# Kernel optimization log

Hardware: AMD Instinct MI355X
Metric: run time of the kernel (lower is better)

The kernel has to match this reference:

```python
import math
import jax, jax.numpy as jnp
import numpy as np

FNUM = 64      # exp_channels (fnum)
NHEADS = 4     # num_heads
WS = 8         # window size (both spatial dims)
SHIFT = 4      # cyclic shift (hard-coded in module)
SCALE = FNUM ** -0.5   # NOTE: module scales by fnum**-0.5, not head_dim**-0.5
LN_EPS = 1e-5


def sine_pos_encoding(h, w, num_pos_feats, temperature=10000.0):
    # DETR-style normalized sine position encoding -> (1, h*w, 2*num_pos_feats)
    scale = 2.0 * math.pi
    y = np.cumsum(np.ones((1, h, w), dtype=np.float64), axis=1)
    x = np.cumsum(np.ones((1, h, w), dtype=np.float64), axis=2)
    eps = 1e-6
    y = y / (y[:, -1:, :] + eps) * scale
    x = x / (x[:, :, -1:] + eps) * scale
    dim_t = np.arange(num_pos_feats, dtype=np.float64)
    dim_t = temperature ** (2.0 * (dim_t // 2) / num_pos_feats)
    pos_x = x[..., None] / dim_t
    pos_y = y[..., None] / dim_t
    pos_x = np.stack([np.sin(pos_x[..., 0::2]), np.cos(pos_x[..., 1::2])], axis=-1).reshape(1, h, w, -1)
    pos_y = np.stack([np.sin(pos_y[..., 0::2]), np.cos(pos_y[..., 1::2])], axis=-1).reshape(1, h, w, -1)
    pos = np.concatenate([pos_y, pos_x], axis=-1)
    return jnp.asarray(pos.reshape(1, h * w, 2 * num_pos_feats), dtype=jnp.float32)


def compute_mask_np(H, W, ws, ss):
    # Swin shifted-window attention mask -> (nW, ws*ws, ws*ws) with 0 / -100
    img = np.zeros((H, W))
    cnt = 0
    for hs in (slice(0, -ws), slice(-ws, -ss), slice(-ss, None)):
        for wsl in (slice(0, -ws), slice(-ws, -ss), slice(-ss, None)):
            img[hs, wsl] = cnt
            cnt += 1
    mw = img.reshape(H // ws, ws, W // ws, ws).transpose(0, 2, 1, 3).reshape(-1, ws * ws)
    diff = mw[:, None, :] - mw[:, :, None]
    return jnp.asarray(np.where(diff != 0, -100.0, 0.0), dtype=jnp.float32)


def layernorm(x, w, b):
    m = x.mean(-1, keepdims=True)
    v = x.var(-1, keepdims=True)
    return (x - m) * jax.lax.rsqrt(v + LN_EPS) * w + b


def window_attention(q, k, v, mask):
    # q,k,v: (Bw, nH, N, Ch); mask: (nW, N, N)
    att = jnp.einsum('bhnc,bhmc->bhnm', q * SCALE, k)
    nW, N = mask.shape[0], mask.shape[1]
    att = att.reshape(-1, nW, NHEADS, N, N) + mask[None, :, None]
    att = jax.nn.softmax(att.reshape(-1, NHEADS, N, N), axis=-1)
    out = jnp.einsum('bhnm,bhmc->bnhc', att, v)   # merge heads as (nH C)
    return out.reshape(out.shape[0], N, -1)


def merge_heads(q):
    # (Bw, nH, N, Ch) -> (Bw, N, nH*Ch)
    return q.transpose(0, 2, 1, 3).reshape(q.shape[0], q.shape[2], -1)


def geglu(h, w11, b11, w12, b12, w2, b2):
    return (jax.nn.gelu(h @ w11 + b11, approximate=False) * (h @ w12 + b12)) @ w2 + b2


def reference(x, ln1_w, ln1_b, ln2_w, ln2_b, w_qkv, me_w11, me_b11, me_w12, me_b12, me_w2, me_b2, conv11_w, ff_in_w, ff_dw_w, ff_out_w):
    B, _, C, H, W = x.shape
    nHw, nWw = H // WS, W // WS
    nW = nHw * nWw
    N = WS * WS
    Ch = FNUM // NHEADS
    pos = sine_pos_encoding(WS, WS, FNUM // 2)
    mask = compute_mask_np(H, W, WS, SHIFT)
    x0 = x
    xs = jnp.roll(x, (-SHIFT, -SHIFT), axis=(3, 4))
    # window partition: (B,3,C,H,W) -> (B*3*nW, N, C)
    xw = xs.reshape(B, 3, C, nHw, WS, nWw, WS).transpose(0, 1, 3, 5, 4, 6, 2).reshape(-1, N, C)
    xw = layernorm(xw, ln1_w, ln1_b)
    qkv = (xw + pos) @ w_qkv                                   # (B*3*nW, N, 3F)
    # '(B E nW) W (nP C) -> E nP (B nW) W C'
    qkv = qkv.reshape(B, 3, nW, N, 3, FNUM).transpose(1, 4, 0, 2, 3, 5).reshape(3, 3, B * nW, N, FNUM)
    # '(C nH)' head split: head index is the fast axis (faithful to source)
    qkv = qkv.reshape(3, 3, B * nW, N, Ch, NHEADS).transpose(0, 1, 2, 5, 3, 4)  # (E, P, Bw, nH, N, Ch)
    a1 = window_attention(qkv[1, 0], qkv[0, 1], qkv[0, 2], mask)
    a3 = window_attention(qkv[1, 0], qkv[2, 1], qkv[2, 2], mask)
    a21 = window_attention(qkv[0, 0], qkv[1, 1], qkv[1, 2], mask)
    a21b = window_attention(qkv[0, 0], qkv[2, 1], qkv[2, 2], mask)
    a23 = window_attention(qkv[2, 0], qkv[1, 1], qkv[1, 2], mask)
    a23b = window_attention(qkv[2, 0], qkv[0, 1], qkv[0, 2], mask)
    # keep_query=True path: concat attended features with own query, GEGLU per exposure
    h1 = geglu(jnp.concatenate([a21, a21b, merge_heads(qkv[0, 0])], -1), me_w11[0], me_b11[0], me_w12[0], me_b12[0], me_w2[0], me_b2[0])
    h2 = geglu(jnp.concatenate([a1, a3, merge_heads(qkv[1, 0])], -1), me_w11[1], me_b11[1], me_w12[1], me_b12[1], me_w2[1], me_b2[1])
    h3 = geglu(jnp.concatenate([a23, a23b, merge_heads(qkv[2, 0])], -1), me_w11[2], me_b11[2], me_w12[2], me_b12[2], me_w2[2], me_b2[2])
    xc = jnp.concatenate([h1, h2, h3], 0)                      # (3*B*nW, N, F)
    # window reverse + ffn_dconv 1x1 conv across 3F channels
    xr = xc.reshape(3, B, nHw, nWw, WS, WS, FNUM).transpose(1, 0, 6, 2, 4, 3, 5).reshape(B, 3 * FNUM, H, W)
    xr = jnp.einsum('oi,bihw->bohw', conv11_w, xr).reshape(B, 3, FNUM, H, W)
    xr = jnp.roll(xr, (SHIFT, SHIFT), axis=(3, 4))
    xres = xr + x0
    # FFN: LN over (N C), then GEGLU dwconv FeedForward
    xl = layernorm(xres.transpose(0, 3, 4, 1, 2).reshape(B, H, W, 3 * FNUM), ln2_w, ln2_b)
    xcn = xl.transpose(0, 3, 1, 2)                             # (B, 3F, H, W)
    h = jnp.einsum('oi,bihw->bohw', ff_in_w, xcn)              # (B, 12F, H, W)
    h = jax.lax.conv_general_dilated(h, ff_dw_w[:, None], (1, 1), ((1, 1), (1, 1)),
                                     feature_group_count=h.shape[1],
                                     dimension_numbers=('NCHW', 'OIHW', 'NCHW'))
    g1, g2 = jnp.split(h, 2, axis=1)
    h = jax.nn.gelu(g1, approximate=False) * g2                # (B, 6F, H, W)
    out = jnp.einsum('oi,bihw->bohw', ff_out_w, h).reshape(B, 3, FNUM, H, W)
    return xres + out


def setup_inputs():
    key = jax.random.key(0)
    ks = jax.random.split(key, 10)
    F3, F6, F12 = 3 * FNUM, 6 * FNUM, 12 * FNUM
    def w(k, shape, fan_in):
        return jax.random.normal(k, shape, jnp.float32) * (fan_in ** -0.5)
    return {
        'x': jax.random.normal(ks[0], (1, 3, FNUM, 256, 256), jnp.float32),
        'ln1_w': jnp.ones((FNUM,), jnp.float32),
        'ln1_b': jnp.zeros((FNUM,), jnp.float32),
        'ln2_w': jnp.ones((F3,), jnp.float32),
        'ln2_b': jnp.zeros((F3,), jnp.float32),
        'w_qkv': w(ks[1], (FNUM, F3), FNUM),
        'me_w11': w(ks[2], (3, F3, FNUM), F3),
        'me_b11': jnp.zeros((3, FNUM), jnp.float32),
        'me_w12': w(ks[3], (3, F3, FNUM), F3),
        'me_b12': jnp.zeros((3, FNUM), jnp.float32),
        'me_w2': w(ks[4], (3, FNUM, FNUM), FNUM),
        'me_b2': jnp.zeros((3, FNUM), jnp.float32),
        'conv11_w': w(ks[5], (F3, F3), F3),
        'ff_in_w': w(ks[6], (F12, F3), F3),
        'ff_dw_w': w(ks[7], (F12, 3, 3), 9),
        'ff_out_w': w(ks[8], (F3, F6), F6),
    }
```

## Files before the change

### kernel.cpp

```cpp
#include <hip/hip_runtime.h>
#include <hip/hip_bf16.h>
#include <math.h>

typedef __hip_bfloat16 bf16;
typedef __attribute__((ext_vector_type(8))) short short8;
typedef __attribute__((ext_vector_type(4))) short short4v;
typedef __attribute__((ext_vector_type(4))) float f32x4;

__device__ __forceinline__ float b2f(bf16 v) { return __bfloat162float(v); }
__device__ __forceinline__ bf16 f2b(float v) { return __float2bfloat16(v); }
__device__ __forceinline__ short f2s(float v) { bf16 b = __float2bfloat16(v); return *(short*)&b; }
__device__ __forceinline__ float s2f(short s) { bf16 b = *(bf16*)&s; return __bfloat162float(b); }
__device__ __forceinline__ float gelu_exact(float x) {
  return 0.5f * x * (1.0f + erff(x * 0.7071067811865476f));
}
__device__ __forceinline__ bool detect_f32(const void* ln1w) {
  return *(const unsigned int*)ln1w == 0x3F800000u;
}
__device__ __forceinline__ float ldx(const void* p, int i, bool f32) {
  return f32 ? ((const float*)p)[i] : b2f(((const bf16*)p)[i]);
}
#define MFMA16(a, b, c) __builtin_amdgcn_mfma_f32_16x16x32_bf16((a), (b), (c), 0, 0, 0)

#define OFF_LN1W  0
#define OFF_LN1B  64
#define OFF_LN2W  128
#define OFF_LN2B  320
#define OFF_WQKVT 512
#define OFF_W11T  12800
#define OFF_B11   49664
#define OFF_W12T  49856
#define OFF_B12   86720
#define OFF_W2T   86912
#define OFF_B2    99200
#define OFF_CW    99392
#define OFF_FIW   136256
#define OFF_DWW   283712
#define OFF_FOW   290624

#define QOFF 0
#define KOFF 4352
#define VOFF 9472

__global__ void __launch_bounds__(256) k_convert(
    const void* __restrict__ src, bf16* __restrict__ dst, int n,
    const void* __restrict__ raw) {
  const bool f32 = detect_f32(raw);
  int i = blockIdx.x * 256 + threadIdx.x;
  if (i < n) dst[i] = f2b(ldx(src, i, f32));
}

__global__ void __launch_bounds__(256) k_convT(
    const void* __restrict__ src, bf16* __restrict__ dst, int R, int C, int n,
    const void* __restrict__ raw) {
  const bool f32 = detect_f32(raw);
  int i = blockIdx.x * 256 + threadIdx.x;
  if (i >= n) return;
  int rc = R * C;
  int s = i / rc, rem = i - s * rc;
  int r = rem / C, c = rem - r * C;
  dst[s * rc + c * R + r] = f2b(ldx(src, i, f32));
}

__global__ void __launch_bounds__(256) k_pos(float* __restrict__ posT) {
  int i = blockIdx.x * 256 + threadIdx.x;
  if (i >= 4096) return;
  int t = i >> 6, ch = i & 63;
  int r = t >> 3, c = t & 7;
  int c2 = ch & 31;
  float coord = (ch < 32) ? (float)(r + 1) : (float)(c + 1);
  float base = coord * (6.283185307179586f / 8.000001f);
  int k = c2 >> 1;
  float d = powf(10000.0f, (float)k * (1.0f / 16.0f));
  float a = base / d;
  posT[i] = (c2 & 1) ? cosf(a) : sinf(a);
}

__global__ void __launch_bounds__(256) k_qkv(
    const void* __restrict__ x, const void* __restrict__ raw,
    const bf16* __restrict__ W, const float* __restrict__ posT,
    short* __restrict__ qkvS, int wy0, int NWL) {
  const int wl = blockIdx.x;
  const int wy = wy0 + (wl >> 5), wx = wl & 31;
  const int tid = threadIdx.x;
  const bool xf32 = detect_f32(raw);

  __shared__ alignas(16) short xln[192 * 72];
  __shared__ alignas(16) short qout[13824];
  __shared__ float mu[192], rs[192];

  for (int i = tid; i < 3072; i += 256) {
    int xq = i & 1, ty = (i >> 1) & 7, ch = (i >> 4) & 63, e = i >> 10;
    int y  = (wy * 8 + ty + 4) & 255;
    int xs = (wx * 8 + 4 + xq * 4) & 255;
    size_t gi = ((size_t)(e * 64 + ch) * 256 + y) * 256 + xs;
    float f0, f1, f2, f3;
    if (xf32) {
      f32x4 v4 = *(const f32x4*)((const float*)x + gi);
      f0 = v4[0]; f1 = v4[1]; f2 = v4[2]; f3 = v4[3];
    } else {
      short4v v4 = *(const short4v*)((const bf16*)x + gi);
      f0 = s2f(v4[0]); f1 = s2f(v4[1]); f2 = s2f(v4[2]); f3 = s2f(v4[3]);
    }
    int tb = (e * 64 + ty * 8 + xq * 4) * 72 + ch;
    xln[tb]       = f2s(f0);
    xln[tb + 72]  = f2s(f1);
    xln[tb + 144] = f2s(f2);
    xln[tb + 216] = f2s(f3);
  }
  __syncthreads();
  if (tid < 192) {
    const short* row = xln + tid * 72;
    float s = 0.f, s2 = 0.f;
    #pragma unroll
    for (int k8 = 0; k8 < 8; k8++) {
      short8 v = *(const short8*)(row + k8 * 8);
      #pragma unroll
      for (int j = 0; j < 8; j++) { float f = s2f(v[j]); s += f; s2 += f * f; }
    }
    float m = s * (1.0f / 64.0f);
    float var = s2 * (1.0f / 64.0f) - m * m;
    mu[tid] = m; rs[tid] = rsqrtf(var + 1e-5f);
  }
  __syncthreads();
  for (int u = tid; u < 1536; u += 256) {
    int co = u & 7, t = (u >> 3) & 63, e = u >> 9;
    int idx = (e * 64 + t) * 72 + co * 8;
    short8 xv = *(const short8*)(xln + idx);
    float m = mu[e * 64 + t], rr = rs[e * 64 + t];
    const float* pt = posT + t * 64 + co * 8;
    f32x4 pa = *(const f32x4*)pt;
    f32x4 pb = *(const f32x4*)(pt + 4);
    short8 lw = *(const short8*)(const void*)(W + OFF_LN1W + co * 8);
    short8 lb = *(const short8*)(const void*)(W + OFF_LN1B + co * 8);
    short8 o;
    #pragma unroll
    for (int j = 0; j < 8; j++) {
      float p = (j < 4) ? pa[j] : pb[j - 4];
      o[j] = f2s((s2f(xv[j]) - m) * rr * s2f(lw[j]) + s2f(lb[j]) + p);
    }
    *(short8*)(xln + idx) = o;
  }
  __syncthreads();

  const int lid = tid & 63;
  const int w = tid >> 6;
  const int mrow = lid & 15, q = lid >> 4;
  const int t0 = w * 16 + q * 4;
  const int h = mrow & 3;
  const bf16* wqT = W + OFF_WQKVT;
  for (int e = 0; e < 3; e++) {
    short8 a0 = *(const short8*)(xln + (e * 64 + w * 16 + mrow) * 72 + q * 8);
    short8 a1 = *(const short8*)(xln + (e * 64 + w * 16 + mrow) * 72 + 32 + q * 8);
    for (int nt = 0; nt < 12; nt++) {
      f32x4 acc = {0.f, 0.f, 0.f, 0.f};
      short8 b0 = *(const short8*)(const void*)(wqT + (nt * 16 + mrow) * 64 + q * 8);
      short8 b1 = *(const short8*)(const void*)(wqT + (nt * 16 + mrow) * 64 + 32 + q * 8);
      acc = MFMA16(a0, b0, acc);
      acc = MFMA16(a1, b1, acc);
      int p = nt >> 2;
      int c = (nt & 3) * 4 + (mrow >> 2);
      if (p == 0) {
        int o2 = h * 16 + c;
        #pragma unroll
        for (int r = 0; r < 4; r++)
          qout[QOFF + (t0 + r) * 68 + o2] = f2s(acc[r]);
      } else if (p == 1) {
        int rb = KOFF + (h * 64 + t0) * 20 + c;
        #pragma unroll
        for (int r = 0; r < 4; r++)
          qout[rb + r * 20] = f2s(acc[r] * 0.125f);
      } else {
        int rb = VOFF + (h * 16 + c) * 68 + q * 16 + w;
        #pragma unroll
        for (int r = 0; r < 4; r++)
          qout[rb + r * 4] = f2s(acc[r]);
      }
    }
    __syncthreads();
    const size_t gb = ((size_t)wl * 9 + e * 3) * 4096;
    for (int u = tid; u < 3072; u += 256) {
      int j = u * 4, p = j >> 12, rem = j & 4095, src;
      if (p == 0)      src = QOFF + (rem >> 6) * 68 + (rem & 63);
      else if (p == 1) src = KOFF + (rem >> 4) * 20 + (rem & 15);
      else             src = VOFF + (rem >> 6) * 68 + (rem & 63);
      *(short4v*)(qkvS + gb + j) = *(const short4v*)(qout + src);
    }
    __syncthreads();
  }
}

__global__ void __launch_bounds__(256, 3) k_attn(
    const short* __restrict__ qkvS, const bf16* __restrict__ W,
    short* __restrict__ xcS, int wy0, int NWL) {
  const int e  = blockIdx.x / NWL;
  const int wl = blockIdx.x - e * NWL;
  const int wy = wy0 + (wl >> 5), wx = wl & 31;
  const int tid = threadIdx.x;

  __shared__ alignas(16) short cat[64 * 200];
  __shared__ alignas(16) short Kh[4096];
  __shared__ alignas(16) short Vt[64 * 72];
  __shared__ alignas(16) short Pb[64 * 72];
  __shared__ alignas(16) short kz[16];
  short* gbuf = Pb;

  const int ea = (e == 0) ? 1 : ((e == 1) ? 0 : 1);
  const int eb = (e == 0) ? 2 : ((e == 1) ? 2 : 0);
  const short* Qg = qkvS + ((size_t)wl * 9 + e * 3 + 0) * 4096;
  const short* Kg[2] = { qkvS + ((size_t)wl * 9 + ea * 3 + 1) * 4096,
                         qkvS + ((size_t)wl * 9 + eb * 3 + 1) * 4096 };
  const short* Vg[2] = { qkvS + ((size_t)wl * 9 + ea * 3 + 2) * 4096,
                         qkvS + ((size_t)wl * 9 + eb * 3 + 2) * 4096 };

  if (tid < 16) kz[tid] = 0;
  for (int i = tid; i < 512; i += 256) {
    int t = i >> 3, ch = i & 7;
    *(short8*)(cat + t * 200 + 128 + ch * 8) = *(const short8*)(Qg + t * 64 + ch * 8);
  }

  const int lid = tid & 63;
  const int w = tid >> 6;
  const int mrow = lid & 15, q = lid >> 4;
  const int masky = (wy == 31), maskx = (wx == 31);
  const bool anymask = (masky | maskx) != 0;
  const short8 zero8 = {0, 0, 0, 0, 0, 0, 0, 0};

  float madd[4][4];
  if (anymask) {
    int qi = w * 16 + mrow;
    int lyi = masky ? (((qi >> 3) < 4) ? 1 : 2) : 0;
    int lxi = maskx ? (((qi & 7) < 4) ? 1 : 2) : 0;
    #pragma unroll
    for (int nt = 0; nt < 4; nt++)
      #pragma unroll
      for (int r = 0; r < 4; r++) {
        int kj = nt * 16 + q * 4 + r;
        int lyj = masky ? (((kj >> 3) < 4) ? 1 : 2) : 0;
        int lxj = maskx ? (((kj & 7) < 4) ? 1 : 2) : 0;
        madd[nt][r] = (lyi != lyj || lxi != lxj) ? -100.0f : 0.0f;
      }
  }

  for (int src = 0; src < 2; src++) {
    if (src) __syncthreads();
    for (int i = tid; i < 512; i += 256)
      *(short8*)(Kh + i * 8) = *(const short8*)(Kg[src] + i * 8);
    for (int i = tid; i < 512; i += 256) {
      int row = i >> 3, ch = i & 7;
      *(short8*)(Vt + row * 72 + ch * 8) = *(const short8*)(Vg[src] + row * 64 + ch * 8);
    }
    __syncthreads();

    for (int h = 0; h < 4; h++) {
      short8 qf = (q < 2)
          ? *(const short8*)(cat + (w * 16 + mrow) * 200 + 128 + h * 16 + q * 8)
          : zero8;
      const short* kb; int kstep;
      if (q < 2) { kb = Kh + (h * 64 + mrow) * 16 + q * 8; kstep = 256; }
      else       { kb = kz; kstep = 0; }
      f32x4 s[4];
      #pragma unroll
      for (int nt = 0; nt < 4; nt++) {
        short8 kf = *(const short8*)(kb + nt * kstep);
        f32x4 z = {0.f, 0.f, 0.f, 0.f};
        s[nt] = MFMA16(kf, qf, z);
      }
      if (anymask) {
        #pragma unroll
        for (int nt = 0; nt < 4; nt++)
          #pragma unroll
          for (int r = 0; r < 4; r++) s[nt][r] += madd[nt][r];
      }
      float mx = s[0][0];
      #pragma unroll
      for (int nt = 0; nt < 4; nt++)
        #pragma unroll
        for (int r = 0; r < 4; r++) if (nt | r) mx = fmaxf(mx, s[nt][r]);
      mx = fmaxf(mx, __shfl_xor(mx, 16));
      mx = fmaxf(mx, __shfl_xor(mx, 32));
      float pr[4][4]; float sum = 0.f;
      #pragma unroll
      for (int nt = 0; nt < 4; nt++)
        #pragma unroll
        for (int r = 0; r < 4; r++) {
          float ev = __expf(s[nt][r] - mx);
          pr[nt][r] = ev; sum += ev;
        }
      sum += __shfl_xor(sum, 16);
      sum += __shfl_xor(sum, 32);
      float inv = 1.0f / sum;
      int ro = (w * 16 + mrow) * 72 + q * 16;
      #pragma unroll
      for (int r = 0; r < 4; r++) {
        short4v pv = { f2s(pr[0][r] * inv), f2s(pr[1][r] * inv),
                       f2s(pr[2][r] * inv), f2s(pr[3][r] * inv) };
        *(short4v*)(Pb + ro + r * 4) = pv;
      }
      asm volatile("s_waitcnt lgkmcnt(0)" ::: "memory");
      f32x4 o = {0.f, 0.f, 0.f, 0.f};
      #pragma unroll
      for (int kc = 0; kc < 2; kc++) {
        short8 pa = *(const short8*)(Pb + (w * 16 + mrow) * 72 + kc * 32 + q * 8);
        short8 vb = *(const short8*)(Vt + (h * 16 + mrow) * 72 + kc * 32 + q * 8);
        o = MFMA16(pa, vb, o);
      }
      #pragma unroll
      for (int r = 0; r < 4; r++)
        cat[(w * 16 + q * 4 + r) * 200 + src * 64 + h * 16 + mrow] = f2s(o[r]);
    }
  }
  __syncthreads();

  {
    short8 a[6];
    #pragma unroll
    for (int kc = 0; kc < 6; kc++)
      a[kc] = *(const short8*)(cat + (w * 16 + mrow) * 200 + kc * 32 + q * 8);
    f32x4 ua[4], va[4];
    const bf16* w1T = W + OFF_W11T + (size_t)e * 64 * 192;
    const bf16* w2T = W + OFF_W12T + (size_t)e * 64 * 192;
    for (int nt = 0; nt < 4; nt++) {
      f32x4 au = {0.f, 0.f, 0.f, 0.f}, av = {0.f, 0.f, 0.f, 0.f};
      #pragma unroll
      for (int kc = 0; kc < 6; kc++) {
        short8 bu = *(const short8*)(const void*)(w1T + (nt * 16 + mrow) * 192 + kc * 32 + q * 8);
        short8 bv = *(const short8*)(const void*)(w2T + (nt * 16 + mrow) * 192 + kc * 32 + q * 8);
        au = MFMA16(a[kc], bu, au);
        av = MFMA16(a[kc], bv, av);
      }
      ua[nt] = au; va[nt] = av;
    }
    for (int nt = 0; nt < 4; nt++) {
      int o = nt * 16 + mrow;
      float bu = b2f(W[OFF_B11 + e * 64 + o]);
      float bv = b2f(W[OFF_B12 + e * 64 + o]);
      #pragma unroll
      for (int r = 0; r < 4; r++)
        gbuf[(w * 16 + q * 4 + r) * 72 + o] = f2s(gelu_exact(ua[nt][r] + bu) * (va[nt][r] + bv));
    }
  }
  {
    short8 g0 = *(const short8*)(gbuf + (w * 16 + mrow) * 72 + q * 8);
    short8 g1 = *(const short8*)(gbuf + (w * 16 + mrow) * 72 + 32 + q * 8);
    const bf16* w2T = W + OFF_W2T + (size_t)e * 64 * 64;
    for (int nt = 0; nt < 4; nt++) {
      f32x4 acc = {0.f, 0.f, 0.f, 0.f};
      short8 b0 = *(const short8*)(const void*)(w2T + (nt * 16 + mrow) * 64 + q * 8);
      short8 b1 = *(const short8*)(const void*)(w2T + (nt * 16 + mrow) * 64 + 32 + q * 8);
      acc = MFMA16(g0, b0, acc);
      acc = MFMA16(g1, b1, acc);
      int o = nt * 16 + mrow;
      float bb = b2f(W[OFF_B2 + e * 64 + o]);
      #pragma unroll
      for (int r = 0; r < 4; r++)
        cat[(w * 16 + q * 4 + r) * 200 + o] = f2s(acc[r] + bb);
    }
  }
  __syncthreads();
  short* xcbase = xcS + ((size_t)wl * 3 + e) * 4096;
  for (int i = tid; i < 1024; i += 256) {
    int tt = i >> 4, f4 = (i & 15) * 4;
    *(short4v*)(xcbase + tt * 64 + f4) = *(const short4v*)(cat + tt * 200 + f4);
  }
}

__global__ void __launch_bounds__(256) k_conv11(
    const short* __restrict__ xcS, const bf16* __restrict__ W,
    const void* __restrict__ x, const void* __restrict__ raw,
    short* __restrict__ xres, int wy0, int NWL) {
  const int wl = blockIdx.x;
  const int wy = wy0 + (wl >> 5), wx = wl & 31;
  const int tid = threadIdx.x;
  const bool xf32 = detect_f32(raw);
  __shared__ alignas(16) short ct[64 * 200];
  __shared__ alignas(16) short xt[64 * 200];

  for (int i = tid; i < 3072; i += 256) {
    int e = i >> 10, rem = i & 1023;
    int tt = rem >> 4, f4 = (rem & 15) * 4;
    *(short4v*)(ct + tt * 200 + e * 64 + f4)
        = *(const short4v*)(xcS + ((size_t)wl * 3 + e) * 4096 + tt * 64 + f4);
  }
  for (int i = tid; i < 3072; i += 256) {
    int xq = i & 1, ty = (i >> 1) & 7, ch = (i >> 4) & 63, e = i >> 10;
    int y  = (wy * 8 + ty + 4) & 255;
    int xs = (wx * 8 + 4 + xq * 4) & 255;
    size_t gi = ((size_t)(e * 64 + ch) * 256 + y) * 256 + xs;
    float f0, f1, f2, f3;
    if (xf32) {
      f32x4 v4 = *(const f32x4*)((const float*)x + gi);
      f0 = v4[0]; f1 = v4[1]; f2 = v4[2]; f3 = v4[3];
    } else {
      short4v v4 = *(const short4v*)((const bf16*)x + gi);
      f0 = s2f(v4[0]); f1 = s2f(v4[1]); f2 = s2f(v4[2]); f3 = s2f(v4[3]);
    }
    int tb = (ty * 8 + xq * 4) * 200 + e * 64 + ch;
    xt[tb]       = f2s(f0);
    xt[tb + 200] = f2s(f1);
    xt[tb + 400] = f2s(f2);
    xt[tb + 600] = f2s(f3);
  }
  __syncthreads();

  const int lid = tid & 63;
  const int w = tid >> 6;
  const int mrow = lid & 15, q = lid >> 4;
  short8 a[6];
  #pragma unroll
  for (int kc = 0; kc < 6; kc++)
    a[kc] = *(const short8*)(ct + (w * 16 + mrow) * 200 + kc * 32 + q * 8);
  __syncthreads();

  const bf16* cw = W + OFF_CW;
  for (int nt = 0; nt < 12; nt++) {
    f32x4 acc = {0.f, 0.f, 0.f, 0.f};
    #pragma unroll
    for (int kc = 0; kc < 6; kc++) {
      short8 b = *(const short8*)(const void*)(cw + (nt * 16 + mrow) * 192 + kc * 32 + q * 8);
      acc = MFMA16(a[kc], b, acc);
    }
    int o = nt * 16 + mrow;
    #pragma unroll
    for (int r = 0; r < 4; r++) {
      int t = w * 16 + q * 4 + r;
      ct[t * 200 + o] = f2s(acc[r] + s2f(xt[t * 200 + o]));
    }
  }
  __syncthreads();
  for (int i4 = tid; i4 < 3072; i4 += 256) {
    int t = i4 / 48, o4 = (i4 - t * 48) * 4;
    int y  = (wy * 8 + (t >> 3) + 4) & 255;
    int xx = (wx * 8 + (t & 7) + 4) & 255;
    *(short4v*)(xres + (size_t)(y * 256 + xx) * 192 + o4)
        = *(const short4v*)(ct + t * 200 + o4);
  }
}

__global__ void __launch_bounds__(256) k_ffin(
    const short* __restrict__ xres, const bf16* __restrict__ W,
    short* __restrict__ hS, int y_start, int y0m1) {
  const int y = y_start + (blockIdx.x >> 2);
  const int x0 = (blockIdx.x & 3) * 64;
  const int l = y - y0m1;
  const int tid = threadIdx.x;
  __shared__ alignas(16) short xt[64 * 200];
  __shared__ float mu[64], rs[64];

  for (int i4 = tid; i4 < 3072; i4 += 256) {
    int p = i4 / 48, c4 = (i4 - p * 48) * 4;
    *(short4v*)(xt + p * 200 + c4)
        = *(const short4v*)(xres + (size_t)(y * 256 + x0 + p) * 192 + c4);
  }
  __syncthreads();
  {
    int p = tid >> 2, qd = tid & 3;
    const short* row = xt + p * 200 + qd * 48;
    float s = 0.f, s2 = 0.f;
    #pragma unroll
    for (int k = 0; k < 6; k++) {
      short8 v = *(const short8*)(row + k * 8);
      #pragma unroll
      for (int j = 0; j < 8; j++) { float f = s2f(v[j]); s += f; s2 += f * f; }
    }
    s  += __shfl_xor(s, 1);  s  += __shfl_xor(s, 2);
    s2 += __shfl_xor(s2, 1); s2 += __shfl_xor(s2, 2);
    if (qd == 0) {
      float m = s * (1.0f / 192.0f);
      float var = s2 * (1.0f / 192.0f) - m * m;
      mu[p] = m; rs[p] = rsqrtf(var + 1e-5f);
    }
  }
  __syncthreads();
  for (int i = tid; i < 12288; i += 256) {
    int p = i & 63, ch = i >> 6;
    int idx = p * 200 + ch;
    xt[idx] = f2s((s2f(xt[idx]) - mu[p]) * rs[p] * b2f(W[OFF_LN2W + ch]) + b2f(W[OFF_LN2B + ch]));
  }
  __syncthreads();

  const int lid = tid & 63;
  const int m0 = (tid >> 6) * 16;
  const int mrow = lid & 15, q = lid >> 4;
  short8 a[6];
  #pragma unroll
  for (int kc = 0; kc < 6; kc++)
    a[kc] = *(const short8*)(xt + (m0 + mrow) * 200 + kc * 32 + q * 8);
  __syncthreads();

  const bf16* fiw = W + OFF_FIW;
  for (int c = 0; c < 4; c++) {
    for (int j = 0; j < 12; j++) {
      int nt = c * 12 + j;
      f32x4 acc = {0.f, 0.f, 0.f, 0.f};
      #pragma unroll
      for (int kc = 0; kc < 6; kc++) {
        short8 b = *(const short8*)(const void*)(fiw + (nt * 16 + mrow) * 192 + kc * 32 + q * 8);
        acc = MFMA16(a[kc], b, acc);
      }
      #pragma unroll
      for (int r = 0; r < 4; r++)
        xt[(m0 + q * 4 + r) * 200 + j * 16 + mrow] = f2s(acc[r]);
    }
    __syncthreads();
    for (int i4 = tid; i4 < 3072; i4 += 256) {
      int t = i4 / 48, o4 = (i4 - t * 48) * 4;
      *(short4v*)(hS + (size_t)l * 196608 + (size_t)(x0 + t) * 768 + c * 192 + o4)
          = *(const short4v*)(xt + t * 200 + o4);
    }
    __syncthreads();
  }
}

__global__ void __launch_bounds__(256, 3) k_ffout(
    const short* __restrict__ hS, const bf16* __restrict__ W,
    const short* __restrict__ xres, void* __restrict__ out,
    const void* __restrict__ raw, int y0, int y0m1) {
  const int y = y0 + (blockIdx.x >> 2);
  const int x0 = (blockIdx.x & 3) * 64;
  const int tid = threadIdx.x;
  const bool of32 = detect_f32(raw);
  __shared__ alignas(16) short ga[64 * 392];

  const bf16* dwwT = W + OFF_DWW;
  const int l = y - y0m1;
  const short8 z8 = {0, 0, 0, 0, 0, 0, 0, 0};
  for (int it = 0; it < 3; it++) {
    int unit = it * 256 + tid;
    int pq = unit / 48, oo = unit - pq * 48;
    int o = oo * 8;
    int xxb = x0 + pq * 4;
    float u[4][8], v[4][8];
    #pragma unroll
    for (int t4 = 0; t4 < 4; t4++)
      #pragma unroll
      for (int j = 0; j < 8; j++) { u[t4][j] = 0.f; v[t4][j] = 0.f; }
    #pragma unroll
    for (int dy = -1; dy <= 1; dy++) {
      int yy = y + dy;
      if (yy < 0 || yy >= 256) continue;
      const short* rbase = hS + (size_t)(l + dy) * 196608;
      short8 hu[6], hv[6];
      #pragma unroll
      for (int k = 0; k < 6; k++) {
        int xv = xxb - 1 + k;
        if (xv < 0 || xv >= 256) { hu[k] = z8; hv[k] = z8; }
        else {
          const short* hp = rbase + (size_t)xv * 768 + o;
          hu[k] = *(const short8*)(hp);
          hv[k] = *(const short8*)(hp + 384);
        }
      }
      const bf16* wrow = dwwT + (dy + 1) * 3 * 768 + o;
      short8 w0u = *(const short8*)(const void*)(wrow);
      short8 w0v = *(const short8*)(const void*)(wrow + 384);
      short8 w1u = *(const short8*)(const void*)(wrow + 768);
      short8 w1v = *(const short8*)(const void*)(wrow + 768 + 384);
      short8 w2u = *(const short8*)(const void*)(wrow + 1536);
      short8 w2v = *(const short8*)(const void*)(wrow + 1536 + 384);
      #pragma unroll
      for (int j = 0; j < 8; j++) {
        float a0 = s2f(w0u[j]), a1 = s2f(w1u[j]), a2 = s2f(w2u[j]);
        float b0 = s2f(w0v[j]), b1 = s2f(w1v[j]), b2 = s2f(w2v[j]);
        float fu0 = s2f(hu[0][j]), fu1 = s2f(hu[1][j]), fu2 = s2f(hu[2][j]);
        float fu3 = s2f(hu[3][j]), fu4 = s2f(hu[4][j]), fu5 = s2f(hu[5][j]);
        float fv0 = s2f(hv[0][j]), fv1 = s2f(hv[1][j]), fv2 = s2f(hv[2][j]);
        float fv3 = s2f(hv[3][j]), fv4 = s2f(hv[4][j]), fv5 = s2f(hv[5][j]);
        u[0][j] += a0 * fu0 + a1 * fu1 + a2 * fu2;
        u[1][j] += a0 * fu1 + a1 * fu2 + a2 * fu3;
        u[2][j] += a0 * fu2 + a1 * fu3 + a2 * fu4;
        u[3][j] += a0 * fu3 + a1 * fu4 + a2 * fu5;
        v[0][j] += b0 * fv0 + b1 * fv1 + b2 * fv2;
        v[1][j] += b0 * fv1 + b1 * fv2 + b2 * fv3;
        v[2][j] += b0 * fv2 + b1 * fv3 + b2 * fv4;
        v[3][j] += b0 * fv3 + b1 * fv4 + b2 * fv5;
      }
    }
    #pragma unroll
    for (int t4 = 0; t4 < 4; t4++) {
      short8 g;
      #pragma unroll
      for (int j = 0; j < 8; j++) g[j] = f2s(gelu_exact(u[t4][j]) * v[t4][j]);
      *(short8*)(ga + (pq * 4 + t4) * 392 + o) = g;
    }
  }
  __syncthreads();

  const int lid = tid & 63;
  const int m0 = (tid >> 6) * 16;
  const int mrow = lid & 15, q = lid >> 4;
  short8 a[12];
  #pragma unroll
  for (int kc = 0; kc < 12; kc++)
    a[kc] = *(const short8*)(ga + (m0 + mrow) * 392 + kc * 32 + q * 8);
  __syncthreads();

  for (int i4 = tid; i4 < 3072; i4 += 256) {
    int pp = i4 / 48, c4 = (i4 - pp * 48) * 4;
    *(short4v*)(ga + pp * 392 + 200 + c4)
        = *(const short4v*)(xres + (size_t)(y * 256 + x0 + pp) * 192 + c4);
  }

  const bf16* fow = W + OFF_FOW;
  for (int nt = 0; nt < 12; nt++) {
    f32x4 acc = {0.f, 0.f, 0.f, 0.f};
    #pragma unroll
    for (int kc = 0; kc < 12; kc++) {
      short8 b = *(const short8*)(const void*)(fow + (nt * 16 + mrow) * 384 + kc * 32 + q * 8);
      acc = MFMA16(a[kc], b, acc);
    }
    #pragma unroll
    for (int r = 0; r < 4; r++)
      ga[(m0 + q * 4 + r) * 392 + nt * 16 + mrow] = f2s(acc[r]);
  }
  __syncthreads();

  for (int it = 0; it < 48; it++) {
    int flat = it * 256 + tid;
    int pp = flat & 63, ch = flat >> 6;
    int idx = ch * 65536 + y * 256 + x0 + pp;
    float r = s2f(ga[pp * 392 + ch]) + s2f(ga[pp * 392 + 200 + ch]);
    if (of32) ((float*)out)[idx] = r;
    else      ((bf16*)out)[idx] = f2b(r);
  }
}

extern "C" void kernel_launch(void* const* d_in, const int* in_sizes, int n_in,
                              void* d_out, int out_size, void* d_ws, size_t ws_size,
                              hipStream_t stream) {
  const void* x   = d_in[0];
  const void* raw = d_in[1];
  char* ws = (char*)d_ws;
  bf16*  W    = (bf16*)(ws + 1024);
  float* posT = (float*)(ws + 786432);
  short* xres = (short*)(ws + 0x100000);
  const size_t ATT = 28ull * 1024 * 1024;

  size_t avail = (ws_size > ATT) ? ws_size - ATT : 0;
  int swr = 32;
  while (swr > 1 && (size_t)swr * 3145728ull > avail) swr >>= 1;
  int hr = 256;
  while (hr > 4 && (size_t)(hr + 2) * 393216ull > avail) hr >>= 1;

  short* qkvS = (short*)(ws + ATT);
  short* xcS  = (short*)(ws + ATT + (size_t)swr * 2359296ull);
  short* hS   = (short*)(ws + ATT);

  { const int di[10]   = {1, 2, 3, 4, 7, 9, 11, 12, 13, 15};
    const int offp[10] = {OFF_LN1W, OFF_LN1B, OFF_LN2W, OFF_LN2B, OFF_B11,
                          OFF_B12, OFF_B2, OFF_CW, OFF_FIW, OFF_FOW};
    const int cnt[10]  = {64, 64, 192, 192, 192, 192, 192, 36864, 147456, 73728};
    for (int i = 0; i < 10; i++)
      k_convert<<<(cnt[i] + 255) / 256, 256, 0, stream>>>(
          d_in[di[i]], W + offp[i], cnt[i], raw);
  }
  k_convT<<<(12288 + 255) / 256, 256, 0, stream>>>(d_in[5], W + OFF_WQKVT, 64, 192, 12288, raw);
  k_convT<<<(36864 + 255) / 256, 256, 0, stream>>>(d_in[6], W + OFF_W11T, 192, 64, 36864, raw);
  k_convT<<<(36864 + 255) / 256, 256, 0, stream>>>(d_in[8], W + OFF_W12T, 192, 64, 36864, raw);
  k_convT<<<(12288 + 255) / 256, 256, 0, stream>>>(d_in[10], W + OFF_W2T, 64, 64, 12288, raw);
  k_convT<<<(6912 + 255) / 256, 256, 0, stream>>>(d_in[14], W + OFF_DWW, 768, 9, 6912, raw);
  k_pos<<<16, 256, 0, stream>>>(posT);

  for (int wy0 = 0; wy0 < 32; wy0 += swr) {
    int NWL = swr * 32;
    k_qkv<<<NWL, 256, 0, stream>>>(x, raw, W, posT, qkvS, wy0, NWL);
    k_attn<<<3 * NWL, 256, 0, stream>>>(qkvS, W, xcS, wy0, NWL);
    k_conv11<<<NWL, 256, 0, stream>>>(xcS, W, x, raw, xres, wy0, NWL);
  }

  for (int y0 = 0; y0 < 256; y0 += hr) {
    int ys = (y0 == 0) ? 0 : (y0 - 1);
    int ye = (y0 + hr > 255) ? 255 : (y0 + hr);
    int nrows = ye - ys + 1;
    k_ffin<<<nrows * 4, 256, 0, stream>>>(xres, W, hS, ys, y0 - 1);
    k_ffout<<<hr * 4, 256, 0, stream>>>(hS, W, xres, d_out, raw, y0, y0 - 1);
  }
}
```

Baseline: 757.4 us.

## Use tanh GELU, fp32 depthwise weights, and 2-pixel strips in ffout

Replaces the exact erf GELU with a tanh-approximation built on __expf, in both the MoE gate and the feed-forward output kernel. Depthwise conv weights are now stored as transposed fp32, so bf16 unpacking of weights goes away. The depthwise loop computes 2 output pixels per thread over 6 iterations instead of 4 over 3, which lowers register pressure, and the explicit 3-blocks-per-CU launch bound is dropped. The trade-offs are more redundant halo loads and a GELU approximation that differs slightly from the reference erf form.

```diff
diff --git a/kernel.cpp b/kernel.cpp
--- a/kernel.cpp
+++ b/kernel.cpp
@@ -11,8 +11,11 @@
 __device__ __forceinline__ bf16 f2b(float v) { return __float2bfloat16(v); }
 __device__ __forceinline__ short f2s(float v) { bf16 b = __float2bfloat16(v); return *(short*)&b; }
 __device__ __forceinline__ float s2f(short s) { bf16 b = *(bf16*)&s; return __bfloat162float(b); }
-__device__ __forceinline__ float gelu_exact(float x) {
-  return 0.5f * x * (1.0f + erff(x * 0.7071067811865476f));
+__device__ __forceinline__ float gelu_fast(float x) {
+  float z = 0.7978845608028654f * x * (1.0f + 0.044715f * x * x);
+  float e = __expf(2.0f * z);
+  float t = 1.0f - 2.0f / (e + 1.0f);
+  return 0.5f * x * (1.0f + t);
 }
 __device__ __forceinline__ bool detect_f32(const void* ln1w) {
   return *(const unsigned int*)ln1w == 0x3F800000u;
@@ -35,7 +38,6 @@
 #define OFF_B2    99200
 #define OFF_CW    99392
 #define OFF_FIW   136256
-#define OFF_DWW   283712
 #define OFF_FOW   290624
 
 #define QOFF 0
@@ -60,6 +62,16 @@
   int s = i / rc, rem = i - s * rc;
   int r = rem / C, c = rem - r * C;
   dst[s * rc + c * R + r] = f2b(ldx(src, i, f32));
+}
+
+__global__ void __launch_bounds__(256) k_convTF(
+    const void* __restrict__ src, float* __restrict__ dst, int R, int C, int n,
+    const void* __restrict__ raw) {
+  const bool f32 = detect_f32(raw);
+  int i = blockIdx.x * 256 + threadIdx.x;
+  if (i >= n) return;
+  int r = i / C, c = i - r * C;
+  dst[c * R + r] = ldx(src, i, f32);
 }
 
 __global__ void __launch_bounds__(256) k_pos(float* __restrict__ posT) {
@@ -337,7 +349,7 @@
       float bv = b2f(W[OFF_B12 + e * 64 + o]);
       #pragma unroll
       for (int r = 0; r < 4; r++)
-        gbuf[(w * 16 + q * 4 + r) * 72 + o] = f2s(gelu_exact(ua[nt][r] + bu) * (va[nt][r] + bv));
+        gbuf[(w * 16 + q * 4 + r) * 72 + o] = f2s(gelu_fast(ua[nt][r] + bu) * (va[nt][r] + bv));
     }
   }
   {
@@ -512,8 +524,9 @@
   }
 }
 
-__global__ void __launch_bounds__(256, 3) k_ffout(
+__global__ void __launch_bounds__(256) k_ffout(
     const short* __restrict__ hS, const bf16* __restrict__ W,
+    const float* __restrict__ dwwF,
     const short* __restrict__ xres, void* __restrict__ out,
     const void* __restrict__ raw, int y0, int y0m1) {
   const int y = y0 + (blockIdx.x >> 2);
@@ -522,27 +535,23 @@
   const bool of32 = detect_f32(raw);
   __shared__ alignas(16) short ga[64 * 392];
 
-  const bf16* dwwT = W + OFF_DWW;
   const int l = y - y0m1;
   const short8 z8 = {0, 0, 0, 0, 0, 0, 0, 0};
-  for (int it = 0; it < 3; it++) {
+  for (int it = 0; it < 6; it++) {
     int unit = it * 256 + tid;
     int pq = unit / 48, oo = unit - pq * 48;
     int o = oo * 8;
-    int xxb = x0 + pq * 4;
-    float u[4][8], v[4][8];
-    #pragma unroll
-    for (int t4 = 0; t4 < 4; t4++)
-      #pragma unroll
-      for (int j = 0; j < 8; j++) { u[t4][j] = 0.f; v[t4][j] = 0.f; }
+    int xxb = x0 + pq * 2;
+    float u0[8] = {0,0,0,0,0,0,0,0}, v0[8] = {0,0,0,0,0,0,0,0};
+    float u1[8] = {0,0,0,0,0,0,0,0}, v1[8] = {0,0,0,0,0,0,0,0};
     #pragma unroll
     for (int dy = -1; dy <= 1; dy++) {
       int yy = y + dy;
       if (yy < 0 || yy >= 256) continue;
       const short* rbase = hS + (size_t)(l + dy) * 196608;
-      short8 hu[6], hv[6];
-      #pragma unroll
-      for (int k = 0; k < 6; k++) {
+      short8 hu[4], hv[4];
+      #pragma unroll
+      for (int k = 0; k < 4; k++) {
         int xv = xxb - 1 + k;
         if (xv < 0 || xv >= 256) { hu[k] = z8; hv[k] = z8; }
         else {
@@ -551,38 +560,27 @@
           hv[k] = *(const short8*)(hp + 384);
         }
       }
-      const bf16* wrow = dwwT + (dy + 1) * 3 * 768 + o;
-      short8 w0u = *(const short8*)(const void*)(wrow);
-      short8 w0v = *(const short8*)(const void*)(wrow + 384);
-      short8 w1u = *(const short8*)(const void*)(wrow + 768);
-      short8 w1v = *(const short8*)(const void*)(wrow + 768 + 384);
-      short8 w2u = *(const short8*)(const void*)(wrow + 1536);
-      short8 w2v = *(const short8*)(const void*)(wrow + 1536 + 384);
+      const float* wrow = dwwF + (dy + 1) * 3 * 768 + o;
       #pragma unroll
       for (int j = 0; j < 8; j++) {
-        float a0 = s2f(w0u[j]), a1 = s2f(w1u[j]), a2 = s2f(w2u[j]);
-        float b0 = s2f(w0v[j]), b1 = s2f(w1v[j]), b2 = s2f(w2v[j]);
-        float fu0 = s2f(hu[0][j]), fu1 = s2f(hu[1][j]), fu2 = s2f(hu[2][j]);
-        float fu3 = s2f(hu[3][j]), fu4 = s2f(hu[4][j]), fu5 = s2f(hu[5][j]);
-        float fv0 = s2f(hv[0][j]), fv1 = s2f(hv[1][j]), fv2 = s2f(hv[2][j]);
-        float fv3 = s2f(hv[3][j]), fv4 = s2f(hv[4][j]), fv5 = s2f(hv[5][j]);
-        u[0][j] += a0 * fu0 + a1 * fu1 + a2 * fu2;
-        u[1][j] += a0 * fu1 + a1 * fu2 + a2 * fu3;
-        u[2][j] += a0 * fu2 + a1 * fu3 + a2 * fu4;
-        u[3][j] += a0 * fu3 + a1 * fu4 + a2 * fu5;
-        v[0][j] += b0 * fv0 + b1 * fv1 + b2 * fv2;
-        v[1][j] += b0 * fv1 + b1 * fv2 + b2 * fv3;
-        v[2][j] += b0 * fv2 + b1 * fv3 + b2 * fv4;
-        v[3][j] += b0 * fv3 + b1 * fv4 + b2 * fv5;
-      }
-    }
-    #pragma unroll
-    for (int t4 = 0; t4 < 4; t4++) {
-      short8 g;
-      #pragma unroll
-      for (int j = 0; j < 8; j++) g[j] = f2s(gelu_exact(u[t4][j]) * v[t4][j]);
-      *(short8*)(ga + (pq * 4 + t4) * 392 + o) = g;
-    }
+        float a0 = wrow[j],          a1 = wrow[768 + j],       a2 = wrow[1536 + j];
+        float b0 = wrow[384 + j],    b1 = wrow[768 + 384 + j], b2 = wrow[1536 + 384 + j];
+        float h0u = s2f(hu[0][j]), h1u = s2f(hu[1][j]), h2u = s2f(hu[2][j]), h3u = s2f(hu[3][j]);
+        float h0v = s2f(hv[0][j]), h1v = s2f(hv[1][j]), h2v = s2f(hv[2][j]), h3v = s2f(hv[3][j]);
+        u0[j] += a0 * h0u + a1 * h1u + a2 * h2u;
+        u1[j] += a0 * h1u + a1 * h2u + a2 * h3u;
+        v0[j] += b0 * h0v + b1 * h1v + b2 * h2v;
+        v1[j] += b0 * h1v + b1 * h2v + b2 * h3v;
+      }
+    }
+    short8 g0, g1;
+    #pragma unroll
+    for (int j = 0; j < 8; j++) {
+      g0[j] = f2s(gelu_fast(u0[j]) * v0[j]);
+      g1[j] = f2s(gelu_fast(u1[j]) * v1[j]);
+    }
+    *(short8*)(ga + (pq * 2) * 392 + o)     = g0;
+    *(short8*)(ga + (pq * 2 + 1) * 392 + o) = g1;
   }
   __syncthreads();
 
@@ -633,6 +631,7 @@
   char* ws = (char*)d_ws;
   bf16*  W    = (bf16*)(ws + 1024);
   float* posT = (float*)(ws + 786432);
+  float* dwwF = (float*)(ws + 802816);
   short* xres = (short*)(ws + 0x100000);
   const size_t ATT = 28ull * 1024 * 1024;
 
@@ -658,7 +657,7 @@
   k_convT<<<(36864 + 255) / 256, 256, 0, stream>>>(d_in[6], W + OFF_W11T, 192, 64, 36864, raw);
   k_convT<<<(36864 + 255) / 256, 256, 0, stream>>>(d_in[8], W + OFF_W12T, 192, 64, 36864, raw);
   k_convT<<<(12288 + 255) / 256, 256, 0, stream>>>(d_in[10], W + OFF_W2T, 64, 64, 12288, raw);
-  k_convT<<<(6912 + 255) / 256, 256, 0, stream>>>(d_in[14], W + OFF_DWW, 768, 9, 6912, raw);
+  k_convTF<<<(6912 + 255) / 256, 256, 0, stream>>>(d_in[14], dwwF, 768, 9, 6912, raw);
   k_pos<<<16, 256, 0, stream>>>(posT);
 
   for (int wy0 = 0; wy0 < 32; wy0 += swr) {
@@ -673,6 +672,6 @@
     int ye = (y0 + hr > 255) ? 255 : (y0 + hr);
     int nrows = ye - ys + 1;
     k_ffin<<<nrows * 4, 256, 0, stream>>>(xres, W, hS, ys, y0 - 1);
-    k_ffout<<<hr * 4, 256, 0, stream>>>(hS, W, xres, d_out, raw, y0, y0 - 1);
-  }
-}
+    k_ffout<<<hr * 4, 256, 0, stream>>>(hS, W, dwwF, xres, d_out, raw, y0, y0 - 1);
+  }
+}
```

Result: slower. 842.6 us (+11.3%).
